# Kernel optimization log

Measured on AMD Instinct MI355X. Metric: run time of the kernel, lower is better.

Reference implementation:

```python
import jax, jax.numpy as jnp
import numpy as np

NUM_FEATURES = 16
NUM_CLASSES = 4
HIDDEN = 128
NUM_LAYERS = 2
BN_EPS = 1e-5


def setup_inputs() -> dict:
    key = jax.random.key(0)
    ks = jax.random.split(key, 12)
    B, S, N, F, E = 8, 12, 5000, NUM_FEATURES, 40000
    H, L, C = HIDDEN, NUM_LAYERS, NUM_CLASSES
    x_seq = jax.random.normal(ks[0], (B, S, N, F), dtype=jnp.float32)
    edge_index = jax.random.randint(ks[1], (2, E), 0, N, dtype=jnp.int32)
    edge_weight = jax.random.uniform(ks[2], (E,), dtype=jnp.float32)
    def glorot(k, shape):
        fan_in, fan_out = shape[0], shape[-1]
        lim = jnp.sqrt(6.0 / (fan_in + fan_out)).astype(jnp.float32)
        return jax.random.uniform(k, shape, jnp.float32, -lim, lim)
    lin_in_W = glorot(ks[3], (F, H))
    lin_in_b = jnp.zeros((H,), jnp.float32)
    # per layer: 3 GCNConvs with weight [(H+H), H]
    convW = glorot(ks[4], (L, 3, 2 * H, H))
    convB = jnp.zeros((L, 3, H), jnp.float32)
    bn_gamma = jnp.ones((H,), jnp.float32)
    bn_beta = jnp.zeros((H,), jnp.float32)
    lin_out_W = glorot(ks[5], (H, C))
    lin_out_b = jnp.zeros((C,), jnp.float32)
    return {
        "x_seq": x_seq, "edge_index": edge_index, "edge_weight": edge_weight,
        "lin_in_W": lin_in_W, "lin_in_b": lin_in_b,
        "convW": convW, "convB": convB,
        "bn_gamma": bn_gamma, "bn_beta": bn_beta,
        "lin_out_W": lin_out_W, "lin_out_b": lin_out_b,
    }


def _batch_static_graph(edge_index, edge_weight, batch_size, num_nodes):
    E = edge_index.shape[1]
    shift = (jnp.arange(batch_size, dtype=edge_index.dtype) * num_nodes)  # [B]
    shift = jnp.repeat(shift, E)  # [B*E]
    bei = jnp.tile(edge_index, (1, batch_size)) + shift[None, :]
    bew = jnp.tile(edge_weight, batch_size)
    return bei, bew


def _gcn_norm(edge_index, edge_weight, num_nodes):
    # PyG GCNConv default: add self-loops (weight 1), sym normalization.
    loop = jnp.arange(num_nodes, dtype=edge_index.dtype)
    row = jnp.concatenate([edge_index[0], loop])
    col = jnp.concatenate([edge_index[1], loop])
    w = jnp.concatenate([edge_weight, jnp.ones((num_nodes,), edge_weight.dtype)])
    deg = jax.ops.segment_sum(w, col, num_segments=num_nodes)
    dis = jnp.where(deg > 0, jax.lax.rsqrt(jnp.where(deg > 0, deg, 1.0)), 0.0)
    norm = dis[row] * w * dis[col]
    return row, col, norm


def reference(x_seq, edge_index, edge_weight, lin_in_W, lin_in_b,
              convW, convB, bn_gamma, bn_beta, lin_out_W, lin_out_b):
    B, S, N, F = x_seq.shape
    H = lin_in_W.shape[1]
    L = convW.shape[0]
    bei, bew = _batch_static_graph(edge_index, edge_weight, B, N)
    total = B * N
    row, col, norm = _gcn_norm(bei, bew, total)
    # [S, total, F]
    xs = jnp.transpose(x_seq, (1, 0, 2, 3)).reshape(S, total, F)

    def gconv(x, W, b):
        xw = x @ W                                # [total, H]
        msg = norm[:, None] * xw[row]             # [E', H]
        return jax.ops.segment_sum(msg, col, num_segments=total) + b

    def step(h_all, x_t):
        x_t = jax.nn.relu(x_t @ lin_in_W + lin_in_b)
        new_h = []
        for l in range(L):
            h = h_all[l]
            combined = jnp.concatenate([x_t, h], axis=1)
            r = jax.nn.sigmoid(gconv(combined, convW[l, 0], convB[l, 0]))
            u = jax.nn.sigmoid(gconv(combined, convW[l, 1], convB[l, 1]))
            combined_r = jnp.concatenate([x_t, r * h], axis=1)
            c = jnp.tanh(gconv(combined_r, convW[l, 2], convB[l, 2]))
            h_new = u * h + (1.0 - u) * c
            new_h.append(h_new)
            x_t = h_new  # dropout is identity in eval mode
        return jnp.stack(new_h), None

    h0 = jnp.zeros((L, total, H), x_seq.dtype)
    h_all, _ = jax.lax.scan(step, h0, xs)
    h_final = h_all[-1]
    # BatchNorm over node dimension (training-mode batch statistics)
    mean = jnp.mean(h_final, axis=0)
    var = jnp.var(h_final, axis=0)
    h_final = (h_final - mean) * jax.lax.rsqrt(var + BN_EPS) * bn_gamma + bn_beta
    h_final = jax.nn.relu(h_final)
    out = h_final @ lin_out_W + lin_out_b            # [total, C]
    out = out.reshape(B, N, -1)
    return jax.nn.log_softmax(out, axis=-1)
```

## Files before the change

### kernel.cpp

```cpp
#include <hip/hip_runtime.h>
#include <cstdint>
#include <cstddef>

#define NN 5000
#define EE 40000
#define BATCH 8
#define SS 12
#define FF 16
#define HH 128
#define TOTAL 40000
#define CC 4


typedef __attribute__((ext_vector_type(8))) short short8;
typedef __attribute__((ext_vector_type(4))) float f32x4;

__device__ __forceinline__ unsigned short f2bf(float f) {
  union { float f; unsigned u; } v; v.f = f;
  unsigned r = v.u + 0x7fff + ((v.u >> 16) & 1);
  return (unsigned short)(r >> 16);
}
__device__ __forceinline__ float bf2f(unsigned short b) {
  union { unsigned u; float f; } v; v.u = ((unsigned)b) << 16;
  return v.f;
}
__device__ __forceinline__ float bflo(unsigned v) {
  union { unsigned u; float f; } x; x.u = v << 16; return x.f;
}
__device__ __forceinline__ float bfhi(unsigned v) {
  union { unsigned u; float f; } x; x.u = v & 0xffff0000u; return x.f;
}
__device__ __forceinline__ void qfma16(float* acc, uint4 qv, float ws) {
  unsigned wd[4] = {qv.x, qv.y, qv.z, qv.w};
#pragma unroll
  for (int d = 0; d < 4; d++) {
#pragma unroll
    for (int k = 0; k < 4; k++) {
      int q = (int)((signed char)(wd[d] >> (8 * k)));
      acc[d * 4 + k] += ws * (float)q;
    }
  }
}

__device__ __forceinline__ void gather_accum(const signed char* __restrict__ Gq,
                                             const float* __restrict__ sc,
                                             int e0, int e1,
                                             const int* __restrict__ csr_src,
                                             const float* __restrict__ csr_w,
                                             const float* __restrict__ dis,
                                             int n, int bb, int fo, float* acc) {
  int lane = (bb << 3) | (fo >> 4);
  int deg = e1 - e0;
  int myi = 0; float myw = 0.f;
  if (lane < deg) {
    myi = csr_src[e0 + lane];
    myw = csr_w[e0 + lane];
  }
  float mys = sc[myi];
  float sn = dis[n]; sn *= sn;
  size_t rowSelf = (size_t)(n << 3) + bb;
#pragma unroll
  for (int k = 0; k < 16; k++) acc[k] = 0.f;
  {
    float ws = sn * sc[n];
    uint4 qv = *(const uint4*)&Gq[rowSelf * 128 + fo];
    qfma16(acc, qv, ws);
  }
  int dmax = deg < 64 ? deg : 64;
  int e = 0;
  for (; e + 3 < dmax; e += 4) {
    int s0 = __shfl(myi, e),     s1 = __shfl(myi, e + 1);
    int s2 = __shfl(myi, e + 2), s3 = __shfl(myi, e + 3);
    uint4 qa = *(const uint4*)&Gq[(((size_t)s0 << 3) + bb) * 128 + fo];
    uint4 qb = *(const uint4*)&Gq[(((size_t)s1 << 3) + bb) * 128 + fo];
    uint4 qc = *(const uint4*)&Gq[(((size_t)s2 << 3) + bb) * 128 + fo];
    uint4 qd = *(const uint4*)&Gq[(((size_t)s3 << 3) + bb) * 128 + fo];
    float w0 = __shfl(myw, e)     * __shfl(mys, e);
    float w1 = __shfl(myw, e + 1) * __shfl(mys, e + 1);
    float w2 = __shfl(myw, e + 2) * __shfl(mys, e + 2);
    float w3 = __shfl(myw, e + 3) * __shfl(mys, e + 3);
    qfma16(acc, qa, w0);
    qfma16(acc, qb, w1);
    qfma16(acc, qc, w2);
    qfma16(acc, qd, w3);
  }
  for (; e < dmax; e++) {
    int s0 = __shfl(myi, e);
    float w0 = __shfl(myw, e) * __shfl(mys, e);
    uint4 qa = *(const uint4*)&Gq[(((size_t)s0 << 3) + bb) * 128 + fo];
    qfma16(acc, qa, w0);
  }
  for (int ee = e0 + 64; ee < e1; ee++) {
    int s0 = csr_src[ee];
    float w0 = csr_w[ee] * sc[s0];
    uint4 qa = *(const uint4*)&Gq[(((size_t)s0 << 3) + bb) * 128 + fo];
    qfma16(acc, qa, w0);
  }
}

__device__ __forceinline__ void gru_combine_store(const float* acc, const float* bp,
                                                  const unsigned short* __restrict__ u_in,
                                                  unsigned short* __restrict__ h_io,
                                                  size_t rowSelf, int fo,
                                                  uint4& o0, uint4& o1) {
  uint4 oo[2];
#pragma unroll
  for (int jj = 0; jj < 2; jj++) {
    uint4 uq = *(const uint4*)&u_in[rowSelf * 128 + fo + 8 * jj];
    uint4 hq = *(const uint4*)&h_io[rowSelf * 128 + fo + 8 * jj];
    float uv[8], hv[8];
    uv[0] = bflo(uq.x); uv[1] = bfhi(uq.x); uv[2] = bflo(uq.y); uv[3] = bfhi(uq.y);
    uv[4] = bflo(uq.z); uv[5] = bfhi(uq.z); uv[6] = bflo(uq.w); uv[7] = bfhi(uq.w);
    hv[0] = bflo(hq.x); hv[1] = bfhi(hq.x); hv[2] = bflo(hq.y); hv[3] = bfhi(hq.y);
    hv[4] = bflo(hq.z); hv[5] = bfhi(hq.z); hv[6] = bflo(hq.w); hv[7] = bfhi(hq.w);
    unsigned ow[4];
#pragma unroll
    for (int d = 0; d < 4; d++) {
      float v0 = acc[8 * jj + 2 * d]     + bp[8 * jj + 2 * d];
      float v1 = acc[8 * jj + 2 * d + 1] + bp[8 * jj + 2 * d + 1];
      float c0 = 1.0f - 2.0f / (__expf(2.0f * v0) + 1.0f);
      float c1 = 1.0f - 2.0f / (__expf(2.0f * v1) + 1.0f);
      float n0 = uv[2 * d] * hv[2 * d] + (1.0f - uv[2 * d]) * c0;
      float n1 = uv[2 * d + 1] * hv[2 * d + 1] + (1.0f - uv[2 * d + 1]) * c1;
      ow[d] = (unsigned)f2bf(n0) | ((unsigned)f2bf(n1) << 16);
    }
    oo[jj].x = ow[0]; oo[jj].y = ow[1]; oo[jj].z = ow[2]; oo[jj].w = ow[3];
    *(uint4*)&h_io[rowSelf * 128 + fo + 8 * jj] = oo[jj];
  }
  o0 = oo[0]; o1 = oo[1];
}


__global__ void deg_cnt_kernel(const int* __restrict__ ei, const float* __restrict__ ew,
                               float* __restrict__ deg, int* __restrict__ cnt) {
  int e = blockIdx.x * 256 + threadIdx.x;
  if (e < EE) {
    int col = ei[EE + e];
    atomicAdd(&deg[col], ew[e]);
    atomicAdd(&cnt[col], 1);
  }
}

__global__ void dis_kernel(const float* __restrict__ deg, float* __restrict__ dis) {
  int n = blockIdx.x * 256 + threadIdx.x;
  if (n < NN) dis[n] = rsqrtf(deg[n] + 1.0f);
}

__global__ void scan_kernel(const int* __restrict__ cnt, int* __restrict__ offs) {
  __shared__ int part[256];
  const int CH = (NN + 255) / 256;
  int tid = threadIdx.x;
  int base = tid * CH;
  int s = 0;
  for (int i = 0; i < CH; i++) { int idx = base + i; if (idx < NN) s += cnt[idx]; }
  part[tid] = s;
  __syncthreads();
  for (int off = 1; off < 256; off <<= 1) {
    int v = (tid >= off) ? part[tid - off] : 0;
    __syncthreads();
    part[tid] += v;
    __syncthreads();
  }
  int run = (tid == 0) ? 0 : part[tid - 1];
  for (int i = 0; i < CH; i++) {
    int idx = base + i;
    if (idx < NN) { offs[idx] = run; run += cnt[idx]; }
  }
  if (tid == 255) offs[NN] = run;
}

__global__ void fill_csr_kernel(const int* __restrict__ ei, const float* __restrict__ ew,
                                const float* __restrict__ dis, const int* __restrict__ offs,
                                int* __restrict__ cursor, int* __restrict__ csr_src,
                                float* __restrict__ csr_w) {
  int e = blockIdx.x * 256 + threadIdx.x;
  if (e < EE) {
    int row = ei[e], col = ei[EE + e];
    int pos = offs[col] + atomicAdd(&cursor[col], 1);
    csr_src[pos] = row;
    csr_w[pos] = dis[row] * ew[e] * dis[col];
  }
}


__global__ void prepack_kernel(const float* __restrict__ convW, unsigned short* __restrict__ Wp) {
  int idx = blockIdx.x * 256 + threadIdx.x;
  int lane = idx & 63;
  int ks = (idx >> 6) & 7;
  int nt = (idx >> 9) & 7;
  int g = idx >> 12;
  const float* W = convW + (size_t)g * 256 * 128;
  int n = nt * 16 + (lane & 15);
  int k0 = ks * 32 + (lane >> 4) * 8;
  unsigned short v[8];
#pragma unroll
  for (int j = 0; j < 8; j++) v[j] = f2bf(W[(size_t)(k0 + j) * 128 + n]);
  *(uint4*)(Wp + (size_t)idx * 8) = *(const uint4*)v;
}


__global__ __launch_bounds__(256) void lin_in_kernel(const float* __restrict__ x_seq,
                                                     const float* __restrict__ W,
                                                     const float* __restrict__ b,
                                                     unsigned short* __restrict__ xt, int t) {
  int idx = blockIdx.x * 256 + threadIdx.x;
  int row = idx >> 4, fh = idx & 15;
  int n = row >> 3, bb = row & 7;
  const float* xp = x_seq + (((size_t)bb * SS + t) * NN + n) * FF;
  float4 a0 = *(const float4*)&b[fh * 8];
  float4 a1 = *(const float4*)&b[fh * 8 + 4];
#pragma unroll
  for (int ff = 0; ff < FF; ff++) {
    float xv = xp[ff];
    float4 w0 = *(const float4*)&W[ff * HH + fh * 8];
    float4 w1 = *(const float4*)&W[ff * HH + fh * 8 + 4];
    a0.x += xv * w0.x; a0.y += xv * w0.y; a0.z += xv * w0.z; a0.w += xv * w0.w;
    a1.x += xv * w1.x; a1.y += xv * w1.y; a1.z += xv * w1.z; a1.w += xv * w1.w;
  }
  uint4 o;
  o.x = (unsigned)f2bf(fmaxf(a0.x, 0.f)) | ((unsigned)f2bf(fmaxf(a0.y, 0.f)) << 16);
  o.y = (unsigned)f2bf(fmaxf(a0.z, 0.f)) | ((unsigned)f2bf(fmaxf(a0.w, 0.f)) << 16);
  o.z = (unsigned)f2bf(fmaxf(a1.x, 0.f)) | ((unsigned)f2bf(fmaxf(a1.y, 0.f)) << 16);
  o.w = (unsigned)f2bf(fmaxf(a1.z, 0.f)) | ((unsigned)f2bf(fmaxf(a1.w, 0.f)) << 16);
  *(uint4*)&xt[(size_t)row * 128 + fh * 8] = o;
}


template <int MT, int NTW, int HALVES, int NTHREADS>
__device__ __forceinline__ void gemm_body(const unsigned short* As, float* gmax,
                                          const unsigned short* __restrict__ Wp,
                                          signed char* __restrict__ qA,
                                          signed char* __restrict__ qB,
                                          float* __restrict__ sA,
                                          float* __restrict__ sB,
                                          int rowBase, int tid) {
  constexpr int NWAVES = NTHREADS / 64;
  constexpr int WPG = NWAVES / HALVES;
  static_assert(MT == 2, "node mapping assumes 32-row tile");
  int wv = tid >> 6, lane = tid & 63;
  int m = lane & 15, q = lane >> 4;
  f32x4 acc[MT][NTW];
#pragma unroll
  for (int i = 0; i < MT; i++)
#pragma unroll
    for (int j = 0; j < NTW; j++) acc[i][j] = (f32x4)(0.0f);
  const unsigned short* wbase = Wp + ((size_t)(wv * NTW) * 8 * 64 + lane) * 8;
#pragma unroll
  for (int ks = 0; ks < 8; ks++) {
    short8 a[MT];
#pragma unroll
    for (int mt = 0; mt < MT; mt++)
      a[mt] = *(const short8*)&As[(mt * 16 + m) * 264 + ks * 32 + q * 8];
#pragma unroll
    for (int nt = 0; nt < NTW; nt++) {
      short8 b = *(const short8*)(wbase + (size_t)(nt * 8 + ks) * 64 * 8);
#pragma unroll
      for (int mt = 0; mt < MT; mt++)
        acc[mt][nt] = __builtin_amdgcn_mfma_f32_16x16x32_bf16(a[mt], b, acc[mt][nt], 0, 0, 0);
    }
  }
  float mxa = 0.f, mxb = 0.f;
#pragma unroll
  for (int nt = 0; nt < NTW; nt++)
#pragma unroll
    for (int i = 0; i < 4; i++) {
      mxa = fmaxf(mxa, fabsf(acc[0][nt][i]));
      mxb = fmaxf(mxb, fabsf(acc[1][nt][i]));
    }
#pragma unroll
  for (int off = 16; off; off >>= 1) {
    mxa = fmaxf(mxa, __shfl_down(mxa, off));
    mxb = fmaxf(mxb, __shfl_down(mxb, off));
  }
  if (lane == 0)  { gmax[wv * 4 + 0] = mxa; gmax[wv * 4 + 2] = mxb; }
  if (lane == 32) { gmax[wv * 4 + 1] = mxa; gmax[wv * 4 + 3] = mxb; }
  __syncthreads();
  if (tid < 4 * HALVES) {
    int node = (HALVES == 2) ? (tid >> 1) : tid;
    int half = (HALVES == 2) ? (tid & 1) : 0;
    float g = 0.f;
#pragma unroll
    for (int w = 0; w < WPG; w++) g = fmaxf(g, gmax[(half * WPG + w) * 4 + node]);
    float* sp = half ? sB : sA;
    sp[(rowBase >> 3) + node] = g * (1.0f / 127.0f);
  }
  int half = (HALVES == 2) ? (wv / WPG) : 0;
  int qh = q >> 1;
  float ga = 0.f, gb = 0.f;
#pragma unroll
  for (int w = 0; w < WPG; w++) {
    ga = fmaxf(ga, gmax[(half * WPG + w) * 4 + qh]);
    gb = fmaxf(gb, gmax[(half * WPG + w) * 4 + 2 + qh]);
  }
  float invA = (ga > 0.f) ? (127.0f / ga) : 0.f;
  float invB = (gb > 0.f) ? (127.0f / gb) : 0.f;
  signed char* qbase = (half ? qB : qA);
#pragma unroll
  for (int mt = 0; mt < MT; mt++) {
    float inv = mt ? invB : invA;
#pragma unroll
    for (int nt = 0; nt < NTW; nt++) {
      int colq = (wv * NTW + nt) * 16 + m - half * 128;
      signed char* dst = qbase + (size_t)(rowBase + mt * 16 + q * 4) * 128 + colq;
#pragma unroll
      for (int i = 0; i < 4; i++) {
        int qv = __float2int_rn(acc[mt][nt][i] * inv);
        dst[(size_t)i * 128] = (signed char)qv;
      }
    }
  }
}


template <int NTW, int HALVES>
__global__ __launch_bounds__(512) void gemm_mfma_q(const unsigned short* __restrict__ A1,
                                                   const unsigned short* __restrict__ A2,
                                                   const unsigned short* __restrict__ Wp,
                                                   signed char* __restrict__ qA,
                                                   signed char* __restrict__ qB,
                                                   float* __restrict__ sA,
                                                   float* __restrict__ sB) {
  __shared__ unsigned short As[32 * 264];
  __shared__ float gmax[32];
  int rowBase = blockIdx.x * 32;
  int tid = threadIdx.x;
  for (int c = tid; c < 1024; c += 512) {
    int row = c >> 5; int rest = c & 31; int half = rest >> 4; int sub = rest & 15;
    const unsigned short* src = (half ? A2 : A1) + ((size_t)(rowBase + row) * 128 + sub * 8);
    *(uint4*)&As[row * 264 + half * 128 + sub * 8] = *(const uint4*)src;
  }
  __syncthreads();
  gemm_body<2, NTW, HALVES, 512>(As, gmax, Wp, qA, qB, sA, sB, rowBase, tid);
}


__global__ __launch_bounds__(512, 8) void fused_cand_q(
    const signed char* __restrict__ GqR, const signed char* __restrict__ GqU,
    const float* __restrict__ sR, const float* __restrict__ sU,
    const int* __restrict__ offs, const int* __restrict__ csr_src,
    const float* __restrict__ csr_w, const float* __restrict__ dis,
    const float* __restrict__ bRU, const unsigned short* __restrict__ h,
    unsigned short* __restrict__ u_out,
    const unsigned short* __restrict__ A1, const unsigned short* __restrict__ Wp,
    signed char* __restrict__ Cq, float* __restrict__ sC) {
  __shared__ unsigned short As[32 * 264];
  __shared__ float gmax[32];
  int tid = threadIdx.x;
  int wv = tid >> 6, lane = tid & 63;
  int rowBase = blockIdx.x * 32, gn0 = rowBase >> 3;
  int bb = lane >> 3, fo = (lane & 7) << 4;
  int node8 = wv >> 1, half = wv & 1;
  int n = gn0 + node8;
  int e0 = offs[n], e1 = offs[n + 1];
  {
    int row = tid >> 4, sub = tid & 15;
    *(uint4*)&As[row * 264 + sub * 8] =
        *(const uint4*)&A1[(size_t)(rowBase + row) * 128 + sub * 8];
  }
  float acc[16];
  gather_accum(half ? GqU : GqR, half ? sU : sR, e0, e1, csr_src, csr_w, dis, n, bb, fo, acc);
  const float* bias = bRU + half * 128 + fo;
  size_t rowSelf = ((size_t)n << 3) + bb;
  if (half == 0) {
    int lr = node8 * 8 + bb;
#pragma unroll
    for (int jj = 0; jj < 2; jj++) {
      uint4 hq = *(const uint4*)&h[rowSelf * 128 + fo + 8 * jj];
      float hv[8];
      hv[0] = bflo(hq.x); hv[1] = bfhi(hq.x); hv[2] = bflo(hq.y); hv[3] = bfhi(hq.y);
      hv[4] = bflo(hq.z); hv[5] = bfhi(hq.z); hv[6] = bflo(hq.w); hv[7] = bfhi(hq.w);
      unsigned ow[4];
#pragma unroll
      for (int d = 0; d < 4; d++) {
        float s0 = 1.0f / (1.0f + __expf(-(acc[8 * jj + 2 * d]     + bias[8 * jj + 2 * d])));
        float s1 = 1.0f / (1.0f + __expf(-(acc[8 * jj + 2 * d + 1] + bias[8 * jj + 2 * d + 1])));
        ow[d] = (unsigned)f2bf(s0 * hv[2 * d]) | ((unsigned)f2bf(s1 * hv[2 * d + 1]) << 16);
      }
      uint4 o; o.x = ow[0]; o.y = ow[1]; o.z = ow[2]; o.w = ow[3];
      *(uint4*)&As[lr * 264 + 128 + fo + 8 * jj] = o;
    }
  } else {
#pragma unroll
    for (int jj = 0; jj < 2; jj++) {
      unsigned ow[4];
#pragma unroll
      for (int d = 0; d < 4; d++) {
        float s0 = 1.0f / (1.0f + __expf(-(acc[8 * jj + 2 * d]     + bias[8 * jj + 2 * d])));
        float s1 = 1.0f / (1.0f + __expf(-(acc[8 * jj + 2 * d + 1] + bias[8 * jj + 2 * d + 1])));
        ow[d] = (unsigned)f2bf(s0) | ((unsigned)f2bf(s1) << 16);
      }
      uint4 o; o.x = ow[0]; o.y = ow[1]; o.z = ow[2]; o.w = ow[3];
      *(uint4*)&u_out[rowSelf * 128 + fo + 8 * jj] = o;
    }
  }
  __syncthreads();
  gemm_body<2, 1, 1, 512>(As, gmax, Wp, Cq, Cq, sC, sC, rowBase, tid);
}


__global__ __launch_bounds__(512, 8) void fused_gates_q(
    const signed char* __restrict__ Cq, const float* __restrict__ sC,
    const int* __restrict__ offs, const int* __restrict__ csr_src,
    const float* __restrict__ csr_w, const float* __restrict__ dis,
    const float* __restrict__ bC, const unsigned short* __restrict__ u_in,
    unsigned short* __restrict__ h_io,
    const unsigned short* __restrict__ A2src, const unsigned short* __restrict__ Wp,
    signed char* __restrict__ GqRo, signed char* __restrict__ GqUo,
    float* __restrict__ sRo, float* __restrict__ sUo) {
  __shared__ unsigned short As[32 * 264];
  __shared__ float gmax[32];
  int tid = threadIdx.x;
  int wv = tid >> 6, lane = tid & 63;
  int rowBase = blockIdx.x * 32, gn0 = rowBase >> 3;
  int bb = lane >> 3, fo = (lane & 7) << 4;
  if (wv >= 4) {
    int t2 = tid - 256;
    for (int c = t2; c < 512; c += 256) {
      int row = c >> 4, sub = c & 15;
      *(uint4*)&As[row * 264 + 128 + sub * 8] =
          *(const uint4*)&A2src[(size_t)(rowBase + row) * 128 + sub * 8];
    }
  } else {
    int node8 = wv;
    int n = gn0 + node8;
    int e0 = offs[n], e1 = offs[n + 1];
    float acc[16];
    gather_accum(Cq, sC, e0, e1, csr_src, csr_w, dis, n, bb, fo, acc);
    size_t rowSelf = ((size_t)n << 3) + bb;
    uint4 o0, o1;
    gru_combine_store(acc, bC + fo, u_in, h_io, rowSelf, fo, o0, o1);
    int lr = node8 * 8 + bb;
    *(uint4*)&As[lr * 264 + fo] = o0;
    *(uint4*)&As[lr * 264 + fo + 8] = o1;
  }
  __syncthreads();
  gemm_body<2, 2, 2, 512>(As, gmax, Wp, GqRo, GqUo, sRo, sUo, rowBase, tid);
}


__global__ __launch_bounds__(512, 8) void fused_gates_lin_q(
    const signed char* __restrict__ Cq, const float* __restrict__ sC,
    const int* __restrict__ offs, const int* __restrict__ csr_src,
    const float* __restrict__ csr_w, const float* __restrict__ dis,
    const float* __restrict__ bC, const unsigned short* __restrict__ u_in,
    unsigned short* __restrict__ h_io,
    const float* __restrict__ x_seq, const float* __restrict__ Win,
    const float* __restrict__ bin, unsigned short* __restrict__ xt_out,
    const unsigned short* __restrict__ A2src, const unsigned short* __restrict__ Wp,
    signed char* __restrict__ GqRo, signed char* __restrict__ GqUo,
    float* __restrict__ sRo, float* __restrict__ sUo, int t_next) {
  __shared__ unsigned short As[32 * 264];
  __shared__ float gmax[32];
  int tid = threadIdx.x;
  int wv = tid >> 6, lane = tid & 63;
  int rowBase = blockIdx.x * 32, gn0 = rowBase >> 3;
  int bb = lane >> 3, fo = (lane & 7) << 4;
  if (wv < 4) {
    int node8 = wv;
    int n = gn0 + node8;
    int e0 = offs[n], e1 = offs[n + 1];
    float acc[16];
    gather_accum(Cq, sC, e0, e1, csr_src, csr_w, dis, n, bb, fo, acc);
    size_t rowSelf = ((size_t)n << 3) + bb;
    uint4 o0, o1;
    gru_combine_store(acc, bC + fo, u_in, h_io, rowSelf, fo, o0, o1);
  } else {
    int t2 = tid - 256;
    for (int c = t2; c < 512; c += 256) {
      int row = c >> 4, sub = c & 15;
      *(uint4*)&As[row * 264 + 128 + sub * 8] =
          *(const uint4*)&A2src[(size_t)(rowBase + row) * 128 + sub * 8];
    }
    for (int c = t2; c < 512; c += 256) {
      int row = c >> 4, fh = c & 15;
      int grow = rowBase + row;
      int n2 = grow >> 3, bbv = grow & 7;
      const float* xp = x_seq + (((size_t)bbv * SS + t_next) * NN + n2) * FF;
      float4 a0 = *(const float4*)&bin[fh * 8];
      float4 a1 = *(const float4*)&bin[fh * 8 + 4];
#pragma unroll
      for (int ff = 0; ff < FF; ff++) {
        float xv = xp[ff];
        float4 w0 = *(const float4*)&Win[ff * HH + fh * 8];
        float4 w1 = *(const float4*)&Win[ff * HH + fh * 8 + 4];
        a0.x += xv * w0.x; a0.y += xv * w0.y; a0.z += xv * w0.z; a0.w += xv * w0.w;
        a1.x += xv * w1.x; a1.y += xv * w1.y; a1.z += xv * w1.z; a1.w += xv * w1.w;
      }
      uint4 o;
      o.x = (unsigned)f2bf(fmaxf(a0.x, 0.f)) | ((unsigned)f2bf(fmaxf(a0.y, 0.f)) << 16);
      o.y = (unsigned)f2bf(fmaxf(a0.z, 0.f)) | ((unsigned)f2bf(fmaxf(a0.w, 0.f)) << 16);
      o.z = (unsigned)f2bf(fmaxf(a1.x, 0.f)) | ((unsigned)f2bf(fmaxf(a1.y, 0.f)) << 16);
      o.w = (unsigned)f2bf(fmaxf(a1.z, 0.f)) | ((unsigned)f2bf(fmaxf(a1.w, 0.f)) << 16);
      *(uint4*)&As[row * 264 + fh * 8] = o;
      *(uint4*)&xt_out[(size_t)grow * 128 + fh * 8] = o;
    }
  }
  __syncthreads();
  gemm_body<2, 2, 2, 512>(As, gmax, Wp, GqRo, GqUo, sRo, sUo, rowBase, tid);
}


__global__ __launch_bounds__(256) void scatter_c_update_q(
    const signed char* __restrict__ Cq, const float* __restrict__ sC,
    const int* __restrict__ offs, const int* __restrict__ csr_src,
    const float* __restrict__ csr_w, const float* __restrict__ dis,
    const float* __restrict__ bC, const unsigned short* __restrict__ u,
    unsigned short* __restrict__ h) {
  int tid = threadIdx.x;
  int wv = tid >> 6, lane = tid & 63;
  int n = blockIdx.x * 4 + wv;
  int bb = lane >> 3;
  int fo = (lane & 7) << 4;
  int e0 = offs[n], e1 = offs[n + 1];
  float acc[16];
  gather_accum(Cq, sC, e0, e1, csr_src, csr_w, dis, n, bb, fo, acc);
  size_t rowSelf = (size_t)(n << 3) + bb;
  uint4 o0, o1;
  gru_combine_store(acc, bC + fo, u, h, rowSelf, fo, o0, o1);
}


__global__ __launch_bounds__(256) void bn_stats_kernel(const unsigned short* __restrict__ h,
                                                       float* __restrict__ sums) {
  __shared__ float ls[512];
  int tid = threadIdx.x;
  float s = 0.f, sq = 0.f;
  for (size_t idx = (size_t)blockIdx.x * 256 + tid; idx < (size_t)TOTAL * HH;
       idx += (size_t)gridDim.x * 256) {
    float v = bf2f(h[idx]);
    s += v; sq += v * v;
  }
  ls[tid] = s; ls[256 + tid] = sq;
  __syncthreads();
  if (tid < 128) {
    atomicAdd(&sums[tid], ls[tid] + ls[tid + 128]);
    atomicAdd(&sums[128 + tid], ls[256 + tid] + ls[256 + tid + 128]);
  }
}


__global__ __launch_bounds__(256) void final_kernel(const unsigned short* __restrict__ h,
                                                    const float* __restrict__ sums,
                                                    const float* __restrict__ gamma,
                                                    const float* __restrict__ beta,
                                                    const float* __restrict__ Wout,
                                                    const float* __restrict__ bout,
                                                    float* __restrict__ out) {
  int wid = threadIdx.x >> 6, lane = threadIdx.x & 63;
  int row = blockIdx.x * 4 + wid;
  if (row >= TOTAL) return;
  const float inv = 1.0f / (float)TOTAL;
  float p0 = 0.f, p1 = 0.f, p2 = 0.f, p3 = 0.f;
#pragma unroll
  for (int jj = 0; jj < 2; jj++) {
    int j = lane + jj * 64;
    float mean = sums[j] * inv;
    float var = sums[128 + j] * inv - mean * mean;
    float hn = (bf2f(h[(size_t)row * HH + j]) - mean) * rsqrtf(var + 1e-5f) * gamma[j] + beta[j];
    hn = fmaxf(hn, 0.0f);
    p0 += hn * Wout[j * 4 + 0];
    p1 += hn * Wout[j * 4 + 1];
    p2 += hn * Wout[j * 4 + 2];
    p3 += hn * Wout[j * 4 + 3];
  }
  for (int off = 32; off; off >>= 1) {
    p0 += __shfl_down(p0, off);
    p1 += __shfl_down(p1, off);
    p2 += __shfl_down(p2, off);
    p3 += __shfl_down(p3, off);
  }
  if (lane == 0) {
    p0 += bout[0]; p1 += bout[1]; p2 += bout[2]; p3 += bout[3];
    float m = fmaxf(fmaxf(p0, p1), fmaxf(p2, p3));
    float e = __expf(p0 - m) + __expf(p1 - m) + __expf(p2 - m) + __expf(p3 - m);
    float lse = m + __logf(e);
    int bb = row & 7, n = row >> 3;
    float* o = out + ((size_t)bb * NN + n) * 4;
    o[0] = p0 - lse; o[1] = p1 - lse; o[2] = p2 - lse; o[3] = p3 - lse;
  }
}


extern "C" void kernel_launch(void* const* d_in, const int* in_sizes, int n_in,
                              void* d_out, int out_size, void* d_ws, size_t ws_size,
                              hipStream_t stream) {
  const float* x_seq = (const float*)d_in[0];
  const int* ei      = (const int*)d_in[1];
  const float* ew    = (const float*)d_in[2];
  const float* Win   = (const float*)d_in[3];
  const float* bin   = (const float*)d_in[4];
  const float* convW = (const float*)d_in[5];
  const float* convB = (const float*)d_in[6];
  const float* gamma = (const float*)d_in[7];
  const float* beta  = (const float*)d_in[8];
  const float* Wout  = (const float*)d_in[9];
  const float* bout  = (const float*)d_in[10];
  float* out = (float*)d_out;

  char* ws = (char*)d_ws;
  size_t off = 0;
  auto alloc = [&](size_t bytes) {
    void* p = ws + off;
    off += (bytes + 1023) & ~(size_t)1023;
    return p;
  };
  float* deg     = (float*)alloc(NN * 4);
  float* dis     = (float*)alloc(NN * 4);
  int*   cnt     = (int*)alloc(NN * 4);
  int*   offs    = (int*)alloc((NN + 1) * 4);
  int*   cursor  = (int*)alloc(NN * 4);
  int*   csr_src = (int*)alloc(EE * 4);
  float* csr_w   = (float*)alloc(EE * 4);
  float* sums    = (float*)alloc(256 * 4);
  float* sR      = (float*)alloc(NN * 4);
  float* sU      = (float*)alloc(NN * 4);
  float* sC      = (float*)alloc(NN * 4);
  unsigned short* Wp = (unsigned short*)alloc(6 * 32768 * 2);
  const size_t NH = (size_t)TOTAL * HH;
  unsigned short* h0 = (unsigned short*)alloc(NH * 2);
  unsigned short* h1 = (unsigned short*)alloc(NH * 2);
  unsigned short* xt = (unsigned short*)alloc(NH * 2);
  unsigned short* ub = (unsigned short*)alloc(NH * 2);
  signed char* GqR = (signed char*)alloc(NH);
  signed char* GqU = (signed char*)alloc(NH);
  signed char* Cq  = (signed char*)alloc(NH);

  hipMemsetAsync(deg, 0, NN * 4, stream);
  hipMemsetAsync(cnt, 0, NN * 4, stream);
  hipMemsetAsync(cursor, 0, NN * 4, stream);
  hipMemsetAsync(sums, 0, 256 * 4, stream);
  hipMemsetAsync(h0, 0, NH * 2, stream);
  hipMemsetAsync(h1, 0, NH * 2, stream);

  deg_cnt_kernel<<<(EE + 255) / 256, 256, 0, stream>>>(ei, ew, deg, cnt);
  dis_kernel<<<(NN + 255) / 256, 256, 0, stream>>>(deg, dis);
  scan_kernel<<<1, 256, 0, stream>>>(cnt, offs);
  fill_csr_kernel<<<(EE + 255) / 256, 256, 0, stream>>>(ei, ew, dis, offs, cursor, csr_src, csr_w);
  prepack_kernel<<<24576 / 256, 256, 0, stream>>>(convW, Wp);

  const unsigned short* Wg0 = Wp;
  const unsigned short* Wc0 = Wp + (size_t)2 * 32768;
  const unsigned short* Wg1 = Wp + (size_t)3 * 32768;
  const unsigned short* Wc1 = Wp + (size_t)5 * 32768;
  const float* bRU0 = convB;
  const float* bC0  = convB + 2 * HH;
  const float* bRU1 = convB + 3 * HH;
  const float* bC1  = convB + 5 * HH;

  lin_in_kernel<<<TOTAL * 16 / 256, 256, 0, stream>>>(x_seq, Win, bin, xt, 0);
  gemm_mfma_q<2, 2><<<TOTAL / 32, 512, 0, stream>>>(xt, h0, Wg0, GqR, GqU, sR, sU);

  for (int t = 0; t < SS; t++) {
    fused_cand_q<<<TOTAL / 32, 512, 0, stream>>>(GqR, GqU, sR, sU, offs, csr_src, csr_w,
                                                 dis, bRU0, h0, ub, xt, Wc0, Cq, sC);
    fused_gates_q<<<TOTAL / 32, 512, 0, stream>>>(Cq, sC, offs, csr_src, csr_w, dis,
                                                  bC0, ub, h0, h1, Wg1, GqR, GqU, sR, sU);
    fused_cand_q<<<TOTAL / 32, 512, 0, stream>>>(GqR, GqU, sR, sU, offs, csr_src, csr_w,
                                                 dis, bRU1, h1, ub, h0, Wc1, Cq, sC);
    if (t < SS - 1) {
      fused_gates_lin_q<<<TOTAL / 32, 512, 0, stream>>>(Cq, sC, offs, csr_src, csr_w, dis,
                                                        bC1, ub, h1, x_seq, Win, bin, xt,
                                                        h0, Wg0, GqR, GqU, sR, sU, t + 1);
    } else {
      scatter_c_update_q<<<NN / 4, 256, 0, stream>>>(Cq, sC, offs, csr_src, csr_w,
                                                     dis, bC1, ub, h1);
    }
  }

  bn_stats_kernel<<<256, 256, 0, stream>>>(h1, sums);
  final_kernel<<<TOTAL / 4, 256, 0, stream>>>(h1, sums, gamma, beta, Wout, bout, out);
}
```

Before: 1.515 ms.

## Fuse the recurrent time loop into one persistent cooperative kernel

The 48 per-timestep kernel launches are replaced by a single cooperative persistent kernel. It loops over timesteps and phases, strides tiles across blocks, and separates phases with grid-wide syncs. The goal is to remove launch overhead and inter-kernel gaps. In exchange it adds grid-sync cost, caps resident blocks at occupancy, and drops __restrict__ hints by passing pointers through a struct. Shared-memory reuse across tiles inside a block may also race without an extra barrier. The old multi-launch path is kept as a fallback if the cooperative launch fails.

New measurement: 5.881 ms. 3.88x slower.

```diff
diff --git a/kernel.cpp b/kernel.cpp
--- a/kernel.cpp
+++ b/kernel.cpp
@@ -1,6 +1,9 @@
 #include <hip/hip_runtime.h>
+#include <hip/hip_cooperative_groups.h>
 #include <cstdint>
 #include <cstddef>
+
+namespace cg = cooperative_groups;
 
 #define NN 5000
 #define EE 40000
@@ -10,6 +13,7 @@
 #define HH 128
 #define TOTAL 40000
 #define CC 4
+#define NTILES (TOTAL / 32)
 
 
 typedef __attribute__((ext_vector_type(8))) short short8;
@@ -312,6 +316,214 @@
 }
 
 
+struct CoopParams {
+  const signed char* GqR; const signed char* GqU; signed char* Cq;
+  float* sR; float* sU; float* sC;
+  const int* offs; const int* csr_src; const float* csr_w; const float* dis;
+  const float* convB;
+  unsigned short* h0; unsigned short* h1; unsigned short* xt; unsigned short* ub;
+  const float* x_seq; const float* Win; const float* bin;
+  const unsigned short* Wg0; const unsigned short* Wc0;
+  const unsigned short* Wg1; const unsigned short* Wc1;
+};
+
+
+__device__ __forceinline__ void phase_cand(unsigned short* As, float* gmax,
+    const CoopParams& p, int rowBase,
+    const signed char* GqRg, const signed char* GqUg,
+    const float* sRg, const float* sUg,
+    const float* bRU, const unsigned short* h, unsigned short* u_out,
+    const unsigned short* A1, const unsigned short* Wp) {
+  int tid = threadIdx.x;
+  int wv = tid >> 6, lane = tid & 63;
+  int gn0 = rowBase >> 3;
+  int bb = lane >> 3, fo = (lane & 7) << 4;
+  int node8 = wv >> 1, half = wv & 1;
+  int n = gn0 + node8;
+  int e0 = p.offs[n], e1 = p.offs[n + 1];
+  {
+    int row = tid >> 4, sub = tid & 15;
+    *(uint4*)&As[row * 264 + sub * 8] =
+        *(const uint4*)&A1[(size_t)(rowBase + row) * 128 + sub * 8];
+  }
+  float acc[16];
+  gather_accum(half ? GqUg : GqRg, half ? sUg : sRg, e0, e1, p.csr_src, p.csr_w,
+               p.dis, n, bb, fo, acc);
+  const float* bias = bRU + half * 128 + fo;
+  size_t rowSelf = ((size_t)n << 3) + bb;
+  if (half == 0) {
+    int lr = node8 * 8 + bb;
+#pragma unroll
+    for (int jj = 0; jj < 2; jj++) {
+      uint4 hq = *(const uint4*)&h[rowSelf * 128 + fo + 8 * jj];
+      float hv[8];
+      hv[0] = bflo(hq.x); hv[1] = bfhi(hq.x); hv[2] = bflo(hq.y); hv[3] = bfhi(hq.y);
+      hv[4] = bflo(hq.z); hv[5] = bfhi(hq.z); hv[6] = bflo(hq.w); hv[7] = bfhi(hq.w);
+      unsigned ow[4];
+#pragma unroll
+      for (int d = 0; d < 4; d++) {
+        float s0 = 1.0f / (1.0f + __expf(-(acc[8 * jj + 2 * d]     + bias[8 * jj + 2 * d])));
+        float s1 = 1.0f / (1.0f + __expf(-(acc[8 * jj + 2 * d + 1] + bias[8 * jj + 2 * d + 1])));
+        ow[d] = (unsigned)f2bf(s0 * hv[2 * d]) | ((unsigned)f2bf(s1 * hv[2 * d + 1]) << 16);
+      }
+      uint4 o; o.x = ow[0]; o.y = ow[1]; o.z = ow[2]; o.w = ow[3];
+      *(uint4*)&As[lr * 264 + 128 + fo + 8 * jj] = o;
+    }
+  } else {
+#pragma unroll
+    for (int jj = 0; jj < 2; jj++) {
+      unsigned ow[4];
+#pragma unroll
+      for (int d = 0; d < 4; d++) {
+        float s0 = 1.0f / (1.0f + __expf(-(acc[8 * jj + 2 * d]     + bias[8 * jj + 2 * d])));
+        float s1 = 1.0f / (1.0f + __expf(-(acc[8 * jj + 2 * d + 1] + bias[8 * jj + 2 * d + 1])));
+        ow[d] = (unsigned)f2bf(s0) | ((unsigned)f2bf(s1) << 16);
+      }
+      uint4 o; o.x = ow[0]; o.y = ow[1]; o.z = ow[2]; o.w = ow[3];
+      *(uint4*)&u_out[rowSelf * 128 + fo + 8 * jj] = o;
+    }
+  }
+  __syncthreads();
+  gemm_body<2, 1, 1, 512>(As, gmax, Wp, p.Cq, p.Cq, p.sC, p.sC, rowBase, tid);
+}
+
+__device__ __forceinline__ void phase_gates(unsigned short* As, float* gmax,
+    const CoopParams& p, int rowBase,
+    const float* bC, const unsigned short* u_in, unsigned short* h_io,
+    const unsigned short* A2src, const unsigned short* Wp,
+    signed char* GqRo, signed char* GqUo, float* sRo, float* sUo) {
+  int tid = threadIdx.x;
+  int wv = tid >> 6, lane = tid & 63;
+  int gn0 = rowBase >> 3;
+  int bb = lane >> 3, fo = (lane & 7) << 4;
+  if (wv >= 4) {
+    int t2 = tid - 256;
+    for (int c = t2; c < 512; c += 256) {
+      int row = c >> 4, sub = c & 15;
+      *(uint4*)&As[row * 264 + 128 + sub * 8] =
+          *(const uint4*)&A2src[(size_t)(rowBase + row) * 128 + sub * 8];
+    }
+  } else {
+    int node8 = wv;
+    int n = gn0 + node8;
+    int e0 = p.offs[n], e1 = p.offs[n + 1];
+    float acc[16];
+    gather_accum(p.Cq, p.sC, e0, e1, p.csr_src, p.csr_w, p.dis, n, bb, fo, acc);
+    size_t rowSelf = ((size_t)n << 3) + bb;
+    uint4 o0, o1;
+    gru_combine_store(acc, bC + fo, u_in, h_io, rowSelf, fo, o0, o1);
+    int lr = node8 * 8 + bb;
+    *(uint4*)&As[lr * 264 + fo] = o0;
+    *(uint4*)&As[lr * 264 + fo + 8] = o1;
+  }
+  __syncthreads();
+  gemm_body<2, 2, 2, 512>(As, gmax, Wp, GqRo, GqUo, sRo, sUo, rowBase, tid);
+}
+
+__device__ __forceinline__ void phase_gates_lin(unsigned short* As, float* gmax,
+    const CoopParams& p, int rowBase,
+    const float* bC, const unsigned short* u_in, unsigned short* h_io,
+    const unsigned short* A2src, const unsigned short* Wp,
+    signed char* GqRo, signed char* GqUo, float* sRo, float* sUo, int t_next) {
+  int tid = threadIdx.x;
+  int wv = tid >> 6, lane = tid & 63;
+  int gn0 = rowBase >> 3;
+  int bb = lane >> 3, fo = (lane & 7) << 4;
+  if (wv < 4) {
+    int node8 = wv;
+    int n = gn0 + node8;
+    int e0 = p.offs[n], e1 = p.offs[n + 1];
+    float acc[16];
+    gather_accum(p.Cq, p.sC, e0, e1, p.csr_src, p.csr_w, p.dis, n, bb, fo, acc);
+    size_t rowSelf = ((size_t)n << 3) + bb;
+    uint4 o0, o1;
+    gru_combine_store(acc, bC + fo, u_in, h_io, rowSelf, fo, o0, o1);
+  } else {
+    int t2 = tid - 256;
+    for (int c = t2; c < 512; c += 256) {
+      int row = c >> 4, sub = c & 15;
+      *(uint4*)&As[row * 264 + 128 + sub * 8] =
+          *(const uint4*)&A2src[(size_t)(rowBase + row) * 128 + sub * 8];
+    }
+    for (int c = t2; c < 512; c += 256) {
+      int row = c >> 4, fh = c & 15;
+      int grow = rowBase + row;
+      int n2 = grow >> 3, bbv = grow & 7;
+      const float* xp = p.x_seq + (((size_t)bbv * SS + t_next) * NN + n2) * FF;
+      float4 a0 = *(const float4*)&p.bin[fh * 8];
+      float4 a1 = *(const float4*)&p.bin[fh * 8 + 4];
+#pragma unroll
+      for (int ff = 0; ff < FF; ff++) {
+        float xv = xp[ff];
+        float4 w0 = *(const float4*)&p.Win[ff * HH + fh * 8];
+        float4 w1 = *(const float4*)&p.Win[ff * HH + fh * 8 + 4];
+        a0.x += xv * w0.x; a0.y += xv * w0.y; a0.z += xv * w0.z; a0.w += xv * w0.w;
+        a1.x += xv * w1.x; a1.y += xv * w1.y; a1.z += xv * w1.z; a1.w += xv * w1.w;
+      }
+      uint4 o;
+      o.x = (unsigned)f2bf(fmaxf(a0.x, 0.f)) | ((unsigned)f2bf(fmaxf(a0.y, 0.f)) << 16);
+      o.y = (unsigned)f2bf(fmaxf(a0.z, 0.f)) | ((unsigned)f2bf(fmaxf(a0.w, 0.f)) << 16);
+      o.z = (unsigned)f2bf(fmaxf(a1.x, 0.f)) | ((unsigned)f2bf(fmaxf(a1.y, 0.f)) << 16);
+      o.w = (unsigned)f2bf(fmaxf(a1.z, 0.f)) | ((unsigned)f2bf(fmaxf(a1.w, 0.f)) << 16);
+      *(uint4*)&As[row * 264 + fh * 8] = o;
+      *(uint4*)&p.xt[(size_t)grow * 128 + fh * 8] = o;
+    }
+  }
+  __syncthreads();
+  gemm_body<2, 2, 2, 512>(As, gmax, Wp, GqRo, GqUo, sRo, sUo, rowBase, tid);
+}
+
+__device__ __forceinline__ void phase_final(const CoopParams& p, int rowBase,
+    const float* bC, const unsigned short* u_in, unsigned short* h_io) {
+  int tid = threadIdx.x;
+  int wv = tid >> 6, lane = tid & 63;
+  if (wv >= 4) return;
+  int gn0 = rowBase >> 3;
+  int bb = lane >> 3, fo = (lane & 7) << 4;
+  int n = gn0 + wv;
+  int e0 = p.offs[n], e1 = p.offs[n + 1];
+  float acc[16];
+  gather_accum(p.Cq, p.sC, e0, e1, p.csr_src, p.csr_w, p.dis, n, bb, fo, acc);
+  size_t rowSelf = ((size_t)n << 3) + bb;
+  uint4 o0, o1;
+  gru_combine_store(acc, bC + fo, u_in, h_io, rowSelf, fo, o0, o1);
+}
+
+
+__global__ __launch_bounds__(512, 8) void tgcn_loop_kernel(CoopParams p) {
+  __shared__ unsigned short As[32 * 264];
+  __shared__ float gmax[32];
+  cg::grid_group gg = cg::this_grid();
+  const float* bRU0 = p.convB;
+  const float* bC0  = p.convB + 2 * HH;
+  const float* bRU1 = p.convB + 3 * HH;
+  const float* bC1  = p.convB + 5 * HH;
+  for (int t = 0; t < SS; t++) {
+    for (int tile = blockIdx.x; tile < NTILES; tile += gridDim.x)
+      phase_cand(As, gmax, p, tile * 32, p.GqR, p.GqU, p.sR, p.sU, bRU0, p.h0, p.ub,
+                 p.xt, p.Wc0);
+    gg.sync();
+    for (int tile = blockIdx.x; tile < NTILES; tile += gridDim.x)
+      phase_gates(As, gmax, p, tile * 32, bC0, p.ub, p.h0, p.h1, p.Wg1,
+                  (signed char*)p.GqR, (signed char*)p.GqU, p.sR, p.sU);
+    gg.sync();
+    for (int tile = blockIdx.x; tile < NTILES; tile += gridDim.x)
+      phase_cand(As, gmax, p, tile * 32, p.GqR, p.GqU, p.sR, p.sU, bRU1, p.h1, p.ub,
+                 p.h0, p.Wc1);
+    gg.sync();
+    if (t < SS - 1) {
+      for (int tile = blockIdx.x; tile < NTILES; tile += gridDim.x)
+        phase_gates_lin(As, gmax, p, tile * 32, bC1, p.ub, p.h1, p.h0, p.Wg0,
+                        (signed char*)p.GqR, (signed char*)p.GqU, p.sR, p.sU, t + 1);
+      gg.sync();
+    } else {
+      for (int tile = blockIdx.x; tile < NTILES; tile += gridDim.x)
+        phase_final(p, tile * 32, bC1, p.ub, p.h1);
+    }
+  }
+}
+
+
 template <int NTW, int HALVES>
 __global__ __launch_bounds__(512) void gemm_mfma_q(const unsigned short* __restrict__ A1,
                                                    const unsigned short* __restrict__ A2,
@@ -335,188 +547,34 @@
 
 
 __global__ __launch_bounds__(512, 8) void fused_cand_q(
-    const signed char* __restrict__ GqR, const signed char* __restrict__ GqU,
-    const float* __restrict__ sR, const float* __restrict__ sU,
-    const int* __restrict__ offs, const int* __restrict__ csr_src,
-    const float* __restrict__ csr_w, const float* __restrict__ dis,
-    const float* __restrict__ bRU, const unsigned short* __restrict__ h,
-    unsigned short* __restrict__ u_out,
-    const unsigned short* __restrict__ A1, const unsigned short* __restrict__ Wp,
-    signed char* __restrict__ Cq, float* __restrict__ sC) {
+    CoopParams p, const float* bRU, const unsigned short* h,
+    const unsigned short* A1, const unsigned short* Wp) {
   __shared__ unsigned short As[32 * 264];
   __shared__ float gmax[32];
-  int tid = threadIdx.x;
-  int wv = tid >> 6, lane = tid & 63;
-  int rowBase = blockIdx.x * 32, gn0 = rowBase >> 3;
-  int bb = lane >> 3, fo = (lane & 7) << 4;
-  int node8 = wv >> 1, half = wv & 1;
-  int n = gn0 + node8;
-  int e0 = offs[n], e1 = offs[n + 1];
-  {
-    int row = tid >> 4, sub = tid & 15;
-    *(uint4*)&As[row * 264 + sub * 8] =
-        *(const uint4*)&A1[(size_t)(rowBase + row) * 128 + sub * 8];
-  }
-  float acc[16];
-  gather_accum(half ? GqU : GqR, half ? sU : sR, e0, e1, csr_src, csr_w, dis, n, bb, fo, acc);
-  const float* bias = bRU + half * 128 + fo;
-  size_t rowSelf = ((size_t)n << 3) + bb;
-  if (half == 0) {
-    int lr = node8 * 8 + bb;
-#pragma unroll
-    for (int jj = 0; jj < 2; jj++) {
-      uint4 hq = *(const uint4*)&h[rowSelf * 128 + fo + 8 * jj];
-      float hv[8];
-      hv[0] = bflo(hq.x); hv[1] = bfhi(hq.x); hv[2] = bflo(hq.y); hv[3] = bfhi(hq.y);
-      hv[4] = bflo(hq.z); hv[5] = bfhi(hq.z); hv[6] = bflo(hq.w); hv[7] = bfhi(hq.w);
-      unsigned ow[4];
-#pragma unroll
-      for (int d = 0; d < 4; d++) {
-        float s0 = 1.0f / (1.0f + __expf(-(acc[8 * jj + 2 * d]     + bias[8 * jj + 2 * d])));
-        float s1 = 1.0f / (1.0f + __expf(-(acc[8 * jj + 2 * d + 1] + bias[8 * jj + 2 * d + 1])));
-        ow[d] = (unsigned)f2bf(s0 * hv[2 * d]) | ((unsigned)f2bf(s1 * hv[2 * d + 1]) << 16);
-      }
-      uint4 o; o.x = ow[0]; o.y = ow[1]; o.z = ow[2]; o.w = ow[3];
-      *(uint4*)&As[lr * 264 + 128 + fo + 8 * jj] = o;
-    }
-  } else {
-#pragma unroll
-    for (int jj = 0; jj < 2; jj++) {
-      unsigned ow[4];
-#pragma unroll
-      for (int d = 0; d < 4; d++) {
-        float s0 = 1.0f / (1.0f + __expf(-(acc[8 * jj + 2 * d]     + bias[8 * jj + 2 * d])));
-        float s1 = 1.0f / (1.0f + __expf(-(acc[8 * jj + 2 * d + 1] + bias[8 * jj + 2 * d + 1])));
-        ow[d] = (unsigned)f2bf(s0) | ((unsigned)f2bf(s1) << 16);
-      }
-      uint4 o; o.x = ow[0]; o.y = ow[1]; o.z = ow[2]; o.w = ow[3];
-      *(uint4*)&u_out[rowSelf * 128 + fo + 8 * jj] = o;
-    }
-  }
-  __syncthreads();
-  gemm_body<2, 1, 1, 512>(As, gmax, Wp, Cq, Cq, sC, sC, rowBase, tid);
-}
-
+  phase_cand(As, gmax, p, blockIdx.x * 32, p.GqR, p.GqU, p.sR, p.sU, bRU, h, p.ub, A1, Wp);
+}
 
 __global__ __launch_bounds__(512, 8) void fused_gates_q(
-    const signed char* __restrict__ Cq, const float* __restrict__ sC,
-    const int* __restrict__ offs, const int* __restrict__ csr_src,
-    const float* __restrict__ csr_w, const float* __restrict__ dis,
-    const float* __restrict__ bC, const unsigned short* __restrict__ u_in,
-    unsigned short* __restrict__ h_io,
-    const unsigned short* __restrict__ A2src, const unsigned short* __restrict__ Wp,
-    signed char* __restrict__ GqRo, signed char* __restrict__ GqUo,
-    float* __restrict__ sRo, float* __restrict__ sUo) {
+    CoopParams p, const float* bC, unsigned short* h_io,
+    const unsigned short* A2src, const unsigned short* Wp) {
   __shared__ unsigned short As[32 * 264];
   __shared__ float gmax[32];
-  int tid = threadIdx.x;
-  int wv = tid >> 6, lane = tid & 63;
-  int rowBase = blockIdx.x * 32, gn0 = rowBase >> 3;
-  int bb = lane >> 3, fo = (lane & 7) << 4;
-  if (wv >= 4) {
-    int t2 = tid - 256;
-    for (int c = t2; c < 512; c += 256) {
-      int row = c >> 4, sub = c & 15;
-      *(uint4*)&As[row * 264 + 128 + sub * 8] =
-          *(const uint4*)&A2src[(size_t)(rowBase + row) * 128 + sub * 8];
-    }
-  } else {
-    int node8 = wv;
-    int n = gn0 + node8;
-    int e0 = offs[n], e1 = offs[n + 1];
-    float acc[16];
-    gather_accum(Cq, sC, e0, e1, csr_src, csr_w, dis, n, bb, fo, acc);
-    size_t rowSelf = ((size_t)n << 3) + bb;
-    uint4 o0, o1;
-    gru_combine_store(acc, bC + fo, u_in, h_io, rowSelf, fo, o0, o1);
-    int lr = node8 * 8 + bb;
-    *(uint4*)&As[lr * 264 + fo] = o0;
-    *(uint4*)&As[lr * 264 + fo + 8] = o1;
-  }
-  __syncthreads();
-  gemm_body<2, 2, 2, 512>(As, gmax, Wp, GqRo, GqUo, sRo, sUo, rowBase, tid);
-}
-
+  phase_gates(As, gmax, p, blockIdx.x * 32, bC, p.ub, h_io, A2src, Wp,
+              (signed char*)p.GqR, (signed char*)p.GqU, p.sR, p.sU);
+}
 
 __global__ __launch_bounds__(512, 8) void fused_gates_lin_q(
-    const signed char* __restrict__ Cq, const float* __restrict__ sC,
-    const int* __restrict__ offs, const int* __restrict__ csr_src,
-    const float* __restrict__ csr_w, const float* __restrict__ dis,
-    const float* __restrict__ bC, const unsigned short* __restrict__ u_in,
-    unsigned short* __restrict__ h_io,
-    const float* __restrict__ x_seq, const float* __restrict__ Win,
-    const float* __restrict__ bin, unsigned short* __restrict__ xt_out,
-    const unsigned short* __restrict__ A2src, const unsigned short* __restrict__ Wp,
-    signed char* __restrict__ GqRo, signed char* __restrict__ GqUo,
-    float* __restrict__ sRo, float* __restrict__ sUo, int t_next) {
+    CoopParams p, const float* bC, unsigned short* h_io,
+    const unsigned short* A2src, const unsigned short* Wp, int t_next) {
   __shared__ unsigned short As[32 * 264];
   __shared__ float gmax[32];
-  int tid = threadIdx.x;
-  int wv = tid >> 6, lane = tid & 63;
-  int rowBase = blockIdx.x * 32, gn0 = rowBase >> 3;
-  int bb = lane >> 3, fo = (lane & 7) << 4;
-  if (wv < 4) {
-    int node8 = wv;
-    int n = gn0 + node8;
-    int e0 = offs[n], e1 = offs[n + 1];
-    float acc[16];
-    gather_accum(Cq, sC, e0, e1, csr_src, csr_w, dis, n, bb, fo, acc);
-    size_t rowSelf = ((size_t)n << 3) + bb;
-    uint4 o0, o1;
-    gru_combine_store(acc, bC + fo, u_in, h_io, rowSelf, fo, o0, o1);
-  } else {
-    int t2 = tid - 256;
-    for (int c = t2; c < 512; c += 256) {
-      int row = c >> 4, sub = c & 15;
-      *(uint4*)&As[row * 264 + 128 + sub * 8] =
-          *(const uint4*)&A2src[(size_t)(rowBase + row) * 128 + sub * 8];
-    }
-    for (int c = t2; c < 512; c += 256) {
-      int row = c >> 4, fh = c & 15;
-      int grow = rowBase + row;
-      int n2 = grow >> 3, bbv = grow & 7;
-      const float* xp = x_seq + (((size_t)bbv * SS + t_next) * NN + n2) * FF;
-      float4 a0 = *(const float4*)&bin[fh * 8];
-      float4 a1 = *(const float4*)&bin[fh * 8 + 4];
-#pragma unroll
-      for (int ff = 0; ff < FF; ff++) {
-        float xv = xp[ff];
-        float4 w0 = *(const float4*)&Win[ff * HH + fh * 8];
-        float4 w1 = *(const float4*)&Win[ff * HH + fh * 8 + 4];
-        a0.x += xv * w0.x; a0.y += xv * w0.y; a0.z += xv * w0.z; a0.w += xv * w0.w;
-        a1.x += xv * w1.x; a1.y += xv * w1.y; a1.z += xv * w1.z; a1.w += xv * w1.w;
-      }
-      uint4 o;
-      o.x = (unsigned)f2bf(fmaxf(a0.x, 0.f)) | ((unsigned)f2bf(fmaxf(a0.y, 0.f)) << 16);
-      o.y = (unsigned)f2bf(fmaxf(a0.z, 0.f)) | ((unsigned)f2bf(fmaxf(a0.w, 0.f)) << 16);
-      o.z = (unsigned)f2bf(fmaxf(a1.x, 0.f)) | ((unsigned)f2bf(fmaxf(a1.y, 0.f)) << 16);
-      o.w = (unsigned)f2bf(fmaxf(a1.z, 0.f)) | ((unsigned)f2bf(fmaxf(a1.w, 0.f)) << 16);
-      *(uint4*)&As[row * 264 + fh * 8] = o;
-      *(uint4*)&xt_out[(size_t)grow * 128 + fh * 8] = o;
-    }
-  }
-  __syncthreads();
-  gemm_body<2, 2, 2, 512>(As, gmax, Wp, GqRo, GqUo, sRo, sUo, rowBase, tid);
-}
-
-
-__global__ __launch_bounds__(256) void scatter_c_update_q(
-    const signed char* __restrict__ Cq, const float* __restrict__ sC,
-    const int* __restrict__ offs, const int* __restrict__ csr_src,
-    const float* __restrict__ csr_w, const float* __restrict__ dis,
-    const float* __restrict__ bC, const unsigned short* __restrict__ u,
-    unsigned short* __restrict__ h) {
-  int tid = threadIdx.x;
-  int wv = tid >> 6, lane = tid & 63;
-  int n = blockIdx.x * 4 + wv;
-  int bb = lane >> 3;
-  int fo = (lane & 7) << 4;
-  int e0 = offs[n], e1 = offs[n + 1];
-  float acc[16];
-  gather_accum(Cq, sC, e0, e1, csr_src, csr_w, dis, n, bb, fo, acc);
-  size_t rowSelf = (size_t)(n << 3) + bb;
-  uint4 o0, o1;
-  gru_combine_store(acc, bC + fo, u, h, rowSelf, fo, o0, o1);
+  phase_gates_lin(As, gmax, p, blockIdx.x * 32, bC, p.ub, h_io, A2src, Wp,
+                  (signed char*)p.GqR, (signed char*)p.GqU, p.sR, p.sU, t_next);
+}
+
+__global__ __launch_bounds__(512) void scatter_c_update_q(
+    CoopParams p, const float* bC, unsigned short* h_io) {
+  phase_final(p, blockIdx.x * 32, bC, p.ub, h_io);
 }
 
 
@@ -638,32 +696,46 @@
   fill_csr_kernel<<<(EE + 255) / 256, 256, 0, stream>>>(ei, ew, dis, offs, cursor, csr_src, csr_w);
   prepack_kernel<<<24576 / 256, 256, 0, stream>>>(convW, Wp);
 
-  const unsigned short* Wg0 = Wp;
-  const unsigned short* Wc0 = Wp + (size_t)2 * 32768;
-  const unsigned short* Wg1 = Wp + (size_t)3 * 32768;
-  const unsigned short* Wc1 = Wp + (size_t)5 * 32768;
+  CoopParams cp;
+  cp.GqR = GqR; cp.GqU = GqU; cp.Cq = Cq;
+  cp.sR = sR; cp.sU = sU; cp.sC = sC;
+  cp.offs = offs; cp.csr_src = csr_src; cp.csr_w = csr_w; cp.dis = dis;
+  cp.convB = convB;
+  cp.h0 = h0; cp.h1 = h1; cp.xt = xt; cp.ub = ub;
+  cp.x_seq = x_seq; cp.Win = Win; cp.bin = bin;
+  cp.Wg0 = Wp;
+  cp.Wc0 = Wp + (size_t)2 * 32768;
+  cp.Wg1 = Wp + (size_t)3 * 32768;
+  cp.Wc1 = Wp + (size_t)5 * 32768;
+
   const float* bRU0 = convB;
   const float* bC0  = convB + 2 * HH;
   const float* bRU1 = convB + 3 * HH;
   const float* bC1  = convB + 5 * HH;
 
   lin_in_kernel<<<TOTAL * 16 / 256, 256, 0, stream>>>(x_seq, Win, bin, xt, 0);
-  gemm_mfma_q<2, 2><<<TOTAL / 32, 512, 0, stream>>>(xt, h0, Wg0, GqR, GqU, sR, sU);
-
-  for (int t = 0; t < SS; t++) {
-    fused_cand_q<<<TOTAL / 32, 512, 0, stream>>>(GqR, GqU, sR, sU, offs, csr_src, csr_w,
-                                                 dis, bRU0, h0, ub, xt, Wc0, Cq, sC);
-    fused_gates_q<<<TOTAL / 32, 512, 0, stream>>>(Cq, sC, offs, csr_src, csr_w, dis,
-                                                  bC0, ub, h0, h1, Wg1, GqR, GqU, sR, sU);
-    fused_cand_q<<<TOTAL / 32, 512, 0, stream>>>(GqR, GqU, sR, sU, offs, csr_src, csr_w,
-                                                 dis, bRU1, h1, ub, h0, Wc1, Cq, sC);
-    if (t < SS - 1) {
-      fused_gates_lin_q<<<TOTAL / 32, 512, 0, stream>>>(Cq, sC, offs, csr_src, csr_w, dis,
-                                                        bC1, ub, h1, x_seq, Win, bin, xt,
-                                                        h0, Wg0, GqR, GqU, sR, sU, t + 1);
-    } else {
-      scatter_c_update_q<<<NN / 4, 256, 0, stream>>>(Cq, sC, offs, csr_src, csr_w,
-                                                     dis, bC1, ub, h1);
+  gemm_mfma_q<2, 2><<<TOTAL / 32, 512, 0, stream>>>(xt, h0, cp.Wg0, GqR, GqU, sR, sU);
+
+  int occ = 0;
+  hipOccupancyMaxActiveBlocksPerMultiprocessor(&occ, tgcn_loop_kernel, 512, 0);
+  int grid = occ * 256;
+  if (grid > NTILES) grid = NTILES;
+  hipError_t cerr = hipErrorUnknown;
+  if (grid >= 64) {
+    void* kargs[] = { (void*)&cp };
+    cerr = hipLaunchCooperativeKernel((void*)tgcn_loop_kernel, dim3(grid), dim3(512),
+                                      kargs, 0, stream);
+  }
+  if (cerr != hipSuccess) {
+    for (int t = 0; t < SS; t++) {
+      fused_cand_q<<<NTILES, 512, 0, stream>>>(cp, bRU0, h0, xt, cp.Wc0);
+      fused_gates_q<<<NTILES, 512, 0, stream>>>(cp, bC0, h0, h1, cp.Wg1);
+      fused_cand_q<<<NTILES, 512, 0, stream>>>(cp, bRU1, h1, h0, cp.Wc1);
+      if (t < SS - 1) {
+        fused_gates_lin_q<<<NTILES, 512, 0, stream>>>(cp, bC1, h1, h0, cp.Wg0, t + 1);
+      } else {
+        scatter_c_update_q<<<NTILES, 512, 0, stream>>>(cp, bC1, h1);
+      }
     }
   }
 
```
